# Kernel tuning notes

Hardware: AMD Instinct MI355X
Metric: run time of the kernel (lower is better)

## Reference

```python
import jax, jax.numpy as jnp
import numpy as np
import math

NINP = 1024
NOUT = 1024
NSLOTS = 15
B = 4096


def setup_inputs() -> dict:
    key = jax.random.key(0)
    ks = jax.random.split(key, 10)
    inp = {
        "input": jax.random.normal(ks[0], (B, NINP), jnp.float32),
        "gate_time": jax.random.uniform(ks[1], (B, NSLOTS), jnp.float32),
        "rmask": jnp.ones((B, NOUT), jnp.float32),
        "memory_h": jax.random.normal(ks[2], (B, NSLOTS, NOUT), jnp.float32),
        "memory_c": jax.random.normal(ks[3], (B, NSLOTS, NOUT), jnp.float32),
        # projector_summ: Linear(ninp+nout, nout) (dropouts are identity in eval)
        "W_proj": jax.random.normal(ks[4], (NOUT, NINP + NOUT), jnp.float32) / np.sqrt(NINP + NOUT),
        "b_proj": jnp.zeros((NOUT,), jnp.float32),
        # LSTMCell(ninp, nout) weights, torch gate order [i, f, g, o]
        "W_ih": jax.random.normal(ks[5], (4 * NOUT, NINP), jnp.float32) / np.sqrt(NINP),
        "W_hh": jax.random.normal(ks[6], (4 * NOUT, NOUT), jnp.float32) / np.sqrt(NOUT),
        "b_ih": jnp.zeros((4 * NOUT,), jnp.float32),
        "b_hh": jnp.zeros((4 * NOUT,), jnp.float32),
    }
    return inp


def reference(input, gate_time, rmask, memory_h, memory_c,
              W_proj, b_proj, W_ih, W_hh, b_ih, b_hh):
    # --- attention over memory slots (gated softmax) ---
    key = jnp.concatenate([input, memory_h[:, 0, :]], axis=1) @ W_proj.T + b_proj  # [B, nout]
    logits = jnp.einsum('bsd,bd->bs', memory_h, key) / math.sqrt(NOUT)             # [B, nslots]
    e = jnp.exp(logits - jnp.max(logits, axis=1, keepdims=True)) * gate_time
    attention = e / jnp.sum(e, axis=1, keepdims=True)
    sel_h = jnp.einsum('bs,bsd->bd', attention, memory_h)
    sel_c = jnp.einsum('bs,bsd->bd', attention, memory_c)

    # --- LSTM cell step (dropout = identity in eval) ---
    gates = input @ W_ih.T + b_ih + (sel_h * rmask) @ W_hh.T + b_hh
    i, f, g, o = jnp.split(gates, 4, axis=1)
    c_i = jax.nn.sigmoid(f) * sel_c + jax.nn.sigmoid(i) * jnp.tanh(g)
    h_i = jax.nn.sigmoid(o) * jnp.tanh(c_i)

    # --- rolling memory update: push new state to slot 0 ---
    memory_h_new = jnp.concatenate([h_i[:, None, :], memory_h[:, :-1, :]], axis=1)
    memory_c_new = jnp.concatenate([c_i[:, None, :], memory_c[:, :-1, :]], axis=1)
    return h_i, memory_h_new, memory_c_new, attention
```

## Files before the change

### kernel.cpp

```cpp
#include <hip/hip_runtime.h>

typedef __attribute__((ext_vector_type(8))) __bf16 bf16x8;
typedef __attribute__((ext_vector_type(4))) float f32x4;
typedef unsigned short u16;
typedef unsigned int u32;

#define NINP 1024
#define NOUT 1024
#define NSLOTS 15
#define BB 4096

__device__ __forceinline__ u16 f2bf(float x) {
  u32 u = __float_as_uint(x);
  u = (u + 0x7FFFu + ((u >> 16) & 1u)) >> 16;
  return (u16)u;
}
__device__ __forceinline__ float bf2f(u16 u) {
  return __uint_as_float(((u32)u) << 16);
}
__device__ __forceinline__ float sigf(float x) {
  return 1.0f / (1.0f + __expf(-x));
}
__device__ __forceinline__ float tanhfast(float x) {
  return 1.0f - 2.0f / (__expf(2.0f * x) + 1.0f);
}

__device__ __forceinline__ void llds16(const u16* g, u16* l) {
  __builtin_amdgcn_global_load_lds(
      (const __attribute__((address_space(1))) void*)g,
      (__attribute__((address_space(3))) void*)l, 16, 0, 0);
}

__global__ void convert_kernel(const float* __restrict__ input,
                               const float* __restrict__ mem_h,
                               const float* __restrict__ W_proj,
                               const float* __restrict__ W_ih,
                               const float* __restrict__ W_hh,
                               u16* __restrict__ X2, u16* __restrict__ WP,
                               u16* __restrict__ WG) {
  const int S0 = 4194304, S1 = 4194304, S2 = 2097152, S3 = 4194304, S4 = 4194304;
  const int total4 = (S0 + S1 + S2 + S3 + S4) >> 2;
  for (int i4 = blockIdx.x * blockDim.x + threadIdx.x; i4 < total4;
       i4 += gridDim.x * blockDim.x) {
    int i = i4 << 2;
    const float* src;
    u16* dst;
    if (i < S0) {
      int j = i, b = j >> 10, d = j & 1023;
      src = input + j;
      dst = X2 + ((size_t)b << 11) + d;
    } else if (i < S0 + S1) {
      int j = i - S0, b = j >> 10, d = j & 1023;
      src = mem_h + (size_t)b * (NSLOTS * NOUT) + d;
      dst = X2 + ((size_t)b << 11) + 1024 + d;
    } else if (i < S0 + S1 + S2) {
      int j = i - S0 - S1;
      src = W_proj + j;
      dst = WP + j;
    } else if (i < S0 + S1 + S2 + S3) {
      int j = i - S0 - S1 - S2, n = j >> 10, k = j & 1023;
      src = W_ih + j;
      dst = WG + ((size_t)n << 11) + k;
    } else {
      int j = i - S0 - S1 - S2 - S3, n = j >> 10, k = j & 1023;
      src = W_hh + j;
      dst = WG + ((size_t)n << 11) + 1024 + k;
    }
    float4 v = *(const float4*)src;
    ushort4 o;
    o.x = f2bf(v.x); o.y = f2bf(v.y); o.z = f2bf(v.z); o.w = f2bf(v.w);
    *(ushort4*)dst = o;
  }
}

__global__ __launch_bounds__(256) void gemm_bt(
    const u16* __restrict__ A, const u16* __restrict__ W,
    const float* __restrict__ bias1, const float* __restrict__ bias2,
    float* __restrict__ Cf, u16* __restrict__ Cb, int M, int N, int K) {
  __shared__ u16 sA[2][128 * 32];
  __shared__ u16 sB[2][128 * 32];
  const int t = threadIdx.x;
  const int wave = t >> 6, lane = t & 63;
  const int m0 = blockIdx.y * 128, n0 = blockIdx.x * 128;
  const int wr = (wave >> 1) * 64, wc = (wave & 1) * 64;

  f32x4 acc[4][4] = {};

  const int row0 = t >> 2, col0 = (t & 3) * 8;
  const int row1 = (t + 256) >> 2;
  const u16* Ag0 = A + (size_t)(m0 + row0) * K + col0;
  const u16* Ag1 = A + (size_t)(m0 + row1) * K + col0;
  const u16* Wg0 = W + (size_t)(n0 + row0) * K + col0;
  const u16* Wg1 = W + (size_t)(n0 + row1) * K + col0;
  const int l0 = (wave * 64) * 8;
  const int l1 = (256 + wave * 64) * 8;

  auto stage = [&](int buf, int kt) {
    const int k0 = kt * 32;
    llds16(Ag0 + k0, &sA[buf][l0]);
    llds16(Ag1 + k0, &sA[buf][l1]);
    llds16(Wg0 + k0, &sB[buf][l0]);
    llds16(Wg1 + k0, &sB[buf][l1]);
  };

  const int lrow = lane & 15;
  const int kq = (lane >> 4) * 8;

  const int nk = K / 32;
  stage(0, 0);
  for (int kt = 0; kt < nk; ++kt) {
    __syncthreads();
    if (kt + 1 < nk) stage((kt + 1) & 1, kt + 1);
    const int buf = kt & 1;
    bf16x8 af[4], bfr[4];
#pragma unroll
    for (int mi = 0; mi < 4; ++mi)
      af[mi] = *(const bf16x8*)&sA[buf][(wr + mi * 16 + lrow) * 32 + kq];
#pragma unroll
    for (int ni = 0; ni < 4; ++ni)
      bfr[ni] = *(const bf16x8*)&sB[buf][(wc + ni * 16 + lrow) * 32 + kq];
#pragma unroll
    for (int mi = 0; mi < 4; ++mi)
#pragma unroll
      for (int ni = 0; ni < 4; ++ni)
        acc[mi][ni] = __builtin_amdgcn_mfma_f32_16x16x32_bf16(
            af[mi], bfr[ni], acc[mi][ni], 0, 0, 0);
  }

  const int crow = (lane >> 4) * 4;
  const int ccol = lane & 15;
#pragma unroll
  for (int mi = 0; mi < 4; ++mi) {
#pragma unroll
    for (int ni = 0; ni < 4; ++ni) {
      int row = m0 + wr + mi * 16 + crow;
      int col = n0 + wc + ni * 16 + ccol;
      float bv = bias1 ? bias1[col] : 0.0f;
      if (bias2) bv += bias2[col];
#pragma unroll
      for (int r = 0; r < 4; ++r) {
        float v = acc[mi][ni][r] + bv;
        if (Cb)
          Cb[(size_t)(row + r) * N + col] = f2bf(v);
        else
          Cf[(size_t)(row + r) * N + col] = v;
      }
    }
  }
}

__global__ __launch_bounds__(256) void attn_kernel(
    const float* __restrict__ mem_h, const float* __restrict__ mem_c,
    const float* __restrict__ key, const float* __restrict__ gate_time,
    const float* __restrict__ rmask, float* __restrict__ out_mh,
    float* __restrict__ out_mc, float* __restrict__ out_att,
    u16* __restrict__ X2, float* __restrict__ selc) {
  const int b = blockIdx.x;
  const int t = threadIdx.x;
  const int lane = t & 63, wave = t >> 6;

  const float4* mh4 = (const float4*)(mem_h + (size_t)b * (NSLOTS * NOUT));
  const float4* mc4 = (const float4*)(mem_c + (size_t)b * (NSLOTS * NOUT));
  float4 key4 = ((const float4*)(key + ((size_t)b << 10)))[t];

  float4 h[NSLOTS];
  float lg[NSLOTS];
#pragma unroll
  for (int s = 0; s < NSLOTS; ++s) {
    h[s] = mh4[s * 256 + t];
    lg[s] = h[s].x * key4.x + h[s].y * key4.y + h[s].z * key4.z + h[s].w * key4.w;
  }

  __shared__ float red[NSLOTS][4];
#pragma unroll
  for (int s = 0; s < NSLOTS; ++s) {
    float v = lg[s];
    v += __shfl_xor(v, 32); v += __shfl_xor(v, 16); v += __shfl_xor(v, 8);
    v += __shfl_xor(v, 4);  v += __shfl_xor(v, 2);  v += __shfl_xor(v, 1);
    if (lane == 0) red[s][wave] = v;
  }
  __syncthreads();

  float att[NSLOTS];
  float mx = -1e30f;
#pragma unroll
  for (int s = 0; s < NSLOTS; ++s) {
    float v = red[s][0] + red[s][1] + red[s][2] + red[s][3];
    att[s] = v * 0.03125f;
    mx = fmaxf(mx, att[s]);
  }
  float ssum = 0.0f;
#pragma unroll
  for (int s = 0; s < NSLOTS; ++s) {
    att[s] = __expf(att[s] - mx) * gate_time[b * NSLOTS + s];
    ssum += att[s];
  }
  float inv = 1.0f / ssum;
#pragma unroll
  for (int s = 0; s < NSLOTS; ++s) att[s] *= inv;
  if (t == 0) {
#pragma unroll
    for (int s = 0; s < NSLOTS; ++s) out_att[(size_t)b * NSLOTS + s] = att[s];
  }

  float4 sh = {0, 0, 0, 0};
  float4* omh = (float4*)(out_mh + (size_t)b * (NSLOTS * NOUT));
#pragma unroll
  for (int s = 0; s < NSLOTS; ++s) {
    sh.x += att[s] * h[s].x; sh.y += att[s] * h[s].y;
    sh.z += att[s] * h[s].z; sh.w += att[s] * h[s].w;
    if (s < NSLOTS - 1) omh[(s + 1) * 256 + t] = h[s];
  }
  float4 rm = ((const float4*)(rmask + ((size_t)b << 10)))[t];
  sh.x *= rm.x; sh.y *= rm.y; sh.z *= rm.z; sh.w *= rm.w;
  ushort4 shb;
  shb.x = f2bf(sh.x); shb.y = f2bf(sh.y); shb.z = f2bf(sh.z); shb.w = f2bf(sh.w);
  ((ushort4*)(X2 + ((size_t)b << 11) + 1024))[t] = shb;

  float4 sc = {0, 0, 0, 0};
  float4* omc = (float4*)(out_mc + (size_t)b * (NSLOTS * NOUT));
#pragma unroll
  for (int s = 0; s < NSLOTS; ++s) {
    float4 c = mc4[s * 256 + t];
    sc.x += att[s] * c.x; sc.y += att[s] * c.y;
    sc.z += att[s] * c.z; sc.w += att[s] * c.w;
    if (s < NSLOTS - 1) omc[(s + 1) * 256 + t] = c;
  }
  ((float4*)(selc + ((size_t)b << 10)))[t] = sc;
}

__global__ __launch_bounds__(256) void lstm_ew(const u16* __restrict__ gates,
                                               const float* __restrict__ selc,
                                               float* __restrict__ out_h,
                                               float* __restrict__ out_mh,
                                               float* __restrict__ out_mc) {
  int gid = blockIdx.x * blockDim.x + threadIdx.x;
  int b = gid >> 8, t = gid & 255;
  const ushort4* g = (const ushort4*)(gates + ((size_t)b << 12));
  ushort4 iu = g[t], fu = g[256 + t], gu = g[512 + t], ou = g[768 + t];
  float4 sc = ((const float4*)(selc + ((size_t)b << 10)))[t];

  float4 cv, hv;
  {
    float i0 = sigf(bf2f(iu.x)), f0 = sigf(bf2f(fu.x));
    float g0 = tanhfast(bf2f(gu.x)), o0 = sigf(bf2f(ou.x));
    cv.x = f0 * sc.x + i0 * g0; hv.x = o0 * tanhfast(cv.x);
  }
  {
    float i0 = sigf(bf2f(iu.y)), f0 = sigf(bf2f(fu.y));
    float g0 = tanhfast(bf2f(gu.y)), o0 = sigf(bf2f(ou.y));
    cv.y = f0 * sc.y + i0 * g0; hv.y = o0 * tanhfast(cv.y);
  }
  {
    float i0 = sigf(bf2f(iu.z)), f0 = sigf(bf2f(fu.z));
    float g0 = tanhfast(bf2f(gu.z)), o0 = sigf(bf2f(ou.z));
    cv.z = f0 * sc.z + i0 * g0; hv.z = o0 * tanhfast(cv.z);
  }
  {
    float i0 = sigf(bf2f(iu.w)), f0 = sigf(bf2f(fu.w));
    float g0 = tanhfast(bf2f(gu.w)), o0 = sigf(bf2f(ou.w));
    cv.w = f0 * sc.w + i0 * g0; hv.w = o0 * tanhfast(cv.w);
  }
  ((float4*)(out_h + ((size_t)b << 10)))[t] = hv;
  ((float4*)(out_mh + (size_t)b * (NSLOTS * NOUT)))[t] = hv;
  ((float4*)(out_mc + (size_t)b * (NSLOTS * NOUT)))[t] = cv;
}

extern "C" void kernel_launch(void* const* d_in, const int* in_sizes, int n_in,
                              void* d_out, int out_size, void* d_ws,
                              size_t ws_size, hipStream_t stream) {
  const float* input = (const float*)d_in[0];
  const float* gate_time = (const float*)d_in[1];
  const float* rmask = (const float*)d_in[2];
  const float* mem_h = (const float*)d_in[3];
  const float* mem_c = (const float*)d_in[4];
  const float* W_proj = (const float*)d_in[5];
  const float* b_proj = (const float*)d_in[6];
  const float* W_ih = (const float*)d_in[7];
  const float* W_hh = (const float*)d_in[8];
  const float* b_ih = (const float*)d_in[9];
  const float* b_hh = (const float*)d_in[10];

  float* out = (float*)d_out;
  float* out_h = out;
  float* out_mh = out + 4194304;
  float* out_mc = out_mh + 62914560;
  float* out_att = out_mc + 62914560;

  char* ws = (char*)d_ws;
  u16* X2 = (u16*)ws;
  u16* WP = (u16*)(ws + 16777216);
  u16* WG = (u16*)(ws + 20971520);
  float* key = (float*)(ws + 37748736);
  float* selc = (float*)(ws + 54525952);
  u16* gates = (u16*)(ws + 71303168);

  convert_kernel<<<2048, 256, 0, stream>>>(input, mem_h, W_proj, W_ih, W_hh, X2,
                                           WP, WG);
  gemm_bt<<<dim3(8, 32), 256, 0, stream>>>(X2, WP, b_proj, nullptr, key,
                                           nullptr, 4096, 1024, 2048);
  attn_kernel<<<4096, 256, 0, stream>>>(mem_h, mem_c, key, gate_time, rmask,
                                        out_mh, out_mc, out_att, X2, selc);
  gemm_bt<<<dim3(32, 32), 256, 0, stream>>>(X2, WG, b_ih, b_hh, nullptr, gates,
                                            4096, 4096, 2048);
  lstm_ew<<<4096, 256, 0, stream>>>(gates, selc, out_h, out_mh, out_mc);
}
```

Measured before the change: 402.8 us.

## Add 256x256-tile double-buffered bf16 MFMA GEMM for the LSTM gates

Replaces the generic GEMM used for the 4096x4096x2048 gate projection with a dedicated kernel. It uses 256x256 output tiles, 512 threads and a 128KB double-buffered LDS pipeline fed by global_load_lds with swizzled addresses. It also remaps block IDs across XCDs and raises wave priority around the MFMA bursts. The larger tiles are meant to increase operand reuse and hide load latency. The costs are heavy LDS and register use, which allow only one block per CU, and a grid of exactly 256 blocks that relies on filling the CUs in a single wave.

Result: faster. 368.9 us (-8.4%).

```diff
diff --git a/kernel.cpp b/kernel.cpp
--- a/kernel.cpp
+++ b/kernel.cpp
@@ -25,7 +25,7 @@
   return 1.0f - 2.0f / (__expf(2.0f * x) + 1.0f);
 }
 
-__device__ __forceinline__ void llds16(const u16* g, u16* l) {
+__device__ __forceinline__ void llds16(const u16* g, const u16* l) {
   __builtin_amdgcn_global_load_lds(
       (const __attribute__((address_space(1))) void*)g,
       (__attribute__((address_space(3))) void*)l, 16, 0, 0);
@@ -149,6 +149,117 @@
   }
 }
 
+__global__ __launch_bounds__(512, 2) void gemm256(
+    const u16* __restrict__ A, const u16* __restrict__ W,
+    const float* __restrict__ bias1, const float* __restrict__ bias2,
+    u16* __restrict__ Cb, int M, int N, int K) {
+  extern __shared__ __align__(16) u16 smem[];
+  u16* sA = smem;
+  u16* sB = smem + 32768;
+
+  const int t = threadIdx.x;
+  const int wid = t >> 6, lane = t & 63;
+  const int nbx = N >> 8;
+  const int nb = (M >> 8) * nbx;
+  const int cpx = nb >> 3;
+  const int bid = blockIdx.x;
+  const int wg = (bid & 7) * cpx + (bid >> 3);
+  const int m0 = (wg / nbx) << 8;
+  const int n0 = (wg % nbx) << 8;
+
+  const int wm = wid >> 2, wn = wid & 3;
+
+  f32x4 acc[8][4] = {};
+
+  const int src_swz = ((lane >> 5) & 1) << 4;
+  const u16* gA[4];
+  const u16* gB[4];
+#pragma unroll
+  for (int j = 0; j < 4; ++j) {
+    int row = (j & 1) * 128 + (t >> 2);
+    int col = (j >> 1) * 32 + ((((t & 3) * 8) ^ src_swz));
+    gA[j] = A + (size_t)(m0 + row) * K + col;
+    gB[j] = W + (size_t)(n0 + row) * K + col;
+  }
+  auto stage = [&](int kt, int buf) {
+    const int ko = kt * 64;
+    const int lb = buf * 16384;
+#pragma unroll
+    for (int j = 0; j < 4; ++j)
+      llds16(gA[j] + ko, sA + lb + (j * 512 + wid * 64) * 8);
+#pragma unroll
+    for (int j = 0; j < 4; ++j)
+      llds16(gB[j] + ko, sB + lb + (j * 512 + wid * 64) * 8);
+  };
+
+  const int lrow = lane & 15;
+  const int lcol = ((lane >> 4) * 8) ^ (((lane >> 3) & 1) << 4);
+  const u16* pA = sA + (wm * 128 + lrow) * 32 + lcol;
+  const u16* pB = sB + (wn * 64 + lrow) * 32 + lcol;
+
+  const int NKT = K >> 6;
+  stage(0, 0);
+  for (int kt = 0; kt < NKT; ++kt) {
+    const int buf = kt & 1;
+    if (kt + 1 < NKT) {
+      stage(kt + 1, buf ^ 1);
+      asm volatile("s_waitcnt vmcnt(8)" ::: "memory");
+      __builtin_amdgcn_sched_barrier(0);
+    } else {
+      asm volatile("s_waitcnt vmcnt(0)" ::: "memory");
+      __builtin_amdgcn_sched_barrier(0);
+    }
+    __builtin_amdgcn_s_barrier();
+
+    const u16* bA = pA + buf * 16384;
+    const u16* bB = pB + buf * 16384;
+
+    bf16x8 bf[4][2];
+#pragma unroll
+    for (int ni = 0; ni < 4; ++ni)
+#pragma unroll
+      for (int ks = 0; ks < 2; ++ks)
+        bf[ni][ks] = *(const bf16x8*)(bB + ks * 8192 + ni * (16 * 32));
+
+#pragma unroll
+    for (int ph = 0; ph < 4; ++ph) {
+      bf16x8 af[2][2];
+#pragma unroll
+      for (int m2 = 0; m2 < 2; ++m2)
+#pragma unroll
+        for (int ks = 0; ks < 2; ++ks)
+          af[m2][ks] =
+              *(const bf16x8*)(bA + ks * 8192 + (ph * 2 + m2) * (16 * 32));
+      __builtin_amdgcn_s_setprio(1);
+#pragma unroll
+      for (int ks = 0; ks < 2; ++ks)
+#pragma unroll
+        for (int m2 = 0; m2 < 2; ++m2)
+#pragma unroll
+          for (int ni = 0; ni < 4; ++ni)
+            acc[ph * 2 + m2][ni] = __builtin_amdgcn_mfma_f32_16x16x32_bf16(
+                af[m2][ks], bf[ni][ks], acc[ph * 2 + m2][ni], 0, 0, 0);
+      __builtin_amdgcn_s_setprio(0);
+      __builtin_amdgcn_s_barrier();
+    }
+  }
+
+  const int crow = (lane >> 4) * 4;
+  const int ccol = lane & 15;
+#pragma unroll
+  for (int mi = 0; mi < 8; ++mi) {
+#pragma unroll
+    for (int ni = 0; ni < 4; ++ni) {
+      int row = m0 + wm * 128 + mi * 16 + crow;
+      int col = n0 + wn * 64 + ni * 16 + ccol;
+      float bv = bias1[col] + bias2[col];
+#pragma unroll
+      for (int r = 0; r < 4; ++r)
+        Cb[(size_t)(row + r) * N + col] = f2bf(acc[mi][ni][r] + bv);
+    }
+  }
+}
+
 __global__ __launch_bounds__(256) void attn_kernel(
     const float* __restrict__ mem_h, const float* __restrict__ mem_c,
     const float* __restrict__ key, const float* __restrict__ gate_time,
@@ -295,13 +406,16 @@
   float* selc = (float*)(ws + 54525952);
   u16* gates = (u16*)(ws + 71303168);
 
+  (void)hipFuncSetAttribute((const void*)gemm256,
+                            hipFuncAttributeMaxDynamicSharedMemorySize, 131072);
+
   convert_kernel<<<2048, 256, 0, stream>>>(input, mem_h, W_proj, W_ih, W_hh, X2,
                                            WP, WG);
   gemm_bt<<<dim3(8, 32), 256, 0, stream>>>(X2, WP, b_proj, nullptr, key,
                                            nullptr, 4096, 1024, 2048);
   attn_kernel<<<4096, 256, 0, stream>>>(mem_h, mem_c, key, gate_time, rmask,
                                         out_mh, out_mc, out_att, X2, selc);
-  gemm_bt<<<dim3(32, 32), 256, 0, stream>>>(X2, WG, b_ih, b_hh, nullptr, gates,
-                                            4096, 4096, 2048);
+  gemm256<<<256, 512, 131072, stream>>>(X2, WG, b_ih, b_hh, gates, 4096, 4096,
+                                        2048);
   lstm_ew<<<4096, 256, 0, stream>>>(gates, selc, out_h, out_mh, out_mc);
 }
```
